# Performance work log

Measured on AMD Instinct MI355X. Metric: run time of the kernel, lower is better.

## Reference

```python
import jax, jax.numpy as jnp
import numpy as np

N_ATOMS = 4096
N_EDGES = 131072
NUM_BASIS = 8
CUTOFF = 6.0
EMBED = 64      # atom embedding dim
HID = 128       # hidden channel width
SH_DIM = 9      # l=0,1,2 spherical harmonics
TP_IN = HID * SH_DIM  # 1152
N_HEADS = 4
HEAD_DIM = HID // N_HEADS


def _spherical_harmonics(vec):
    # vec: [E,3] -> [E,9] matching the torch SphericalHarmonics (l=0,1,2)
    r = jnp.linalg.norm(vec, axis=-1, keepdims=True) + 1e-8
    u = vec / r
    x, y, z = u[:, 0], u[:, 1], u[:, 2]
    l0 = jnp.ones_like(x)[:, None]
    l1 = jnp.stack([y, z, x], axis=-1)
    l2 = jnp.stack([3.0 * z * z - 1.0, x * z, y * z, x * y, x * x - y * y], axis=-1)
    return jnp.concatenate([l0, l1, l2], axis=-1)


def _rbf(d):
    # bessel RBF with cosine cutoff, d: [E] -> [E, NUM_BASIS]
    freqs = jnp.arange(1, NUM_BASIS + 1, dtype=d.dtype) * (np.pi / CUTOFF)
    cut = 0.5 * (jnp.cos(d * (np.pi / CUTOFF)) + 1.0) * (d < CUTOFF).astype(d.dtype)
    rbf = jnp.sin(d[:, None] * freqs) / d[:, None]
    return rbf * cut[:, None]


def _mace_block(atomic_numbers, edge_index, edge_vectors, edge_lengths,
                atom_embed, rad_w1, rad_b1, rad_w2, rad_b2, tp_w, tp_b,
                msg_w1, msg_b1, msg_w2, msg_b2,
                attn_w_in, attn_b_in, attn_w_out, attn_b_out,
                gate_w, gate_b, out_w, out_b):
    n_atoms = atom_embed.shape[0] if False else atomic_numbers.shape[0]
    node = atom_embed[atomic_numbers]                      # [N,64] gather
    sh = _spherical_harmonics(edge_vectors)                # [E,9]
    rbf = _rbf(edge_lengths)                               # [E,8]
    rad = jax.nn.silu(rbf @ rad_w1 + rad_b1)
    rad = jax.nn.silu(rad @ rad_w2 + rad_b2)               # [E,128]
    # per-l outer products radial x sh_l, flattened channel-major, concatenated
    slices = [(0, 1), (1, 4), (4, 9)]
    msgs = jnp.concatenate(
        [(rad[:, :, None] * sh[:, None, s:e]).reshape(rad.shape[0], -1) for s, e in slices],
        axis=-1)                                           # [E,1152]
    edge_msg = msgs @ tp_w + tp_b                          # [E,128]
    dst = edge_index[1]
    agg = jax.ops.segment_sum(edge_msg, dst, num_segments=n_atoms)  # [N,128] scatter-add
    combined = jnp.concatenate([node, agg], axis=-1)       # [N,192]
    upd = jax.nn.silu(combined @ msg_w1 + msg_b1) @ msg_w2 + msg_b2  # [N,128]
    # multi-head self-attention over all atoms (batch of 1)
    qkv = upd @ attn_w_in.T + attn_b_in                    # [N,384]
    q, k, v = jnp.split(qkv, 3, axis=-1)
    q = q.reshape(-1, N_HEADS, HEAD_DIM)
    k = k.reshape(-1, N_HEADS, HEAD_DIM)
    v = v.reshape(-1, N_HEADS, HEAD_DIM)
    scores = jnp.einsum('nhd,mhd->hnm', q, k) / np.sqrt(HEAD_DIM)
    attn = jax.nn.softmax(scores, axis=-1)
    att = jnp.einsum('hnm,mhd->nhd', attn, v).reshape(-1, HID)
    att = att @ attn_w_out.T + attn_b_out                  # [N,128]
    gate = jax.nn.sigmoid(upd @ gate_w + gate_b)
    out = gate * att + (1.0 - gate) * upd
    return out @ out_w + out_b                             # [N,128]


def setup_inputs() -> dict:
    key = jax.random.key(0)
    ks = jax.random.split(key, 20)
    def w(k, shape, s=0.05):
        return jax.random.normal(k, shape, dtype=jnp.float32) * s
    return {
        'atomic_numbers': jax.random.randint(ks[0], (N_ATOMS,), 0, 100),
        'positions': jax.random.normal(ks[1], (N_ATOMS, 3), dtype=jnp.float32),
        'edge_index': jax.random.randint(ks[2], (2, N_EDGES), 0, N_ATOMS),
        'edge_vectors': jax.random.normal(ks[3], (N_EDGES, 3), dtype=jnp.float32),
        'edge_lengths': jax.random.uniform(ks[4], (N_EDGES,), dtype=jnp.float32, minval=0.5, maxval=5.9),
        'atom_embed': w(ks[5], (100, EMBED), 1.0),
        'rad_w1': w(ks[6], (NUM_BASIS, 64)), 'rad_b1': jnp.zeros((64,), jnp.float32),
        'rad_w2': w(ks[7], (64, HID)), 'rad_b2': jnp.zeros((HID,), jnp.float32),
        'tp_w': w(ks[8], (TP_IN, HID)), 'tp_b': jnp.zeros((HID,), jnp.float32),
        'msg_w1': w(ks[9], (EMBED + HID, HID)), 'msg_b1': jnp.zeros((HID,), jnp.float32),
        'msg_w2': w(ks[10], (HID, HID)), 'msg_b2': jnp.zeros((HID,), jnp.float32),
        'attn_w_in': w(ks[11], (3 * HID, HID)), 'attn_b_in': jnp.zeros((3 * HID,), jnp.float32),
        'attn_w_out': w(ks[12], (HID, HID)), 'attn_b_out': jnp.zeros((HID,), jnp.float32),
        'gate_w': w(ks[13], (HID, HID)), 'gate_b': jnp.zeros((HID,), jnp.float32),
        'out_w': w(ks[14], (HID, HID)), 'out_b': jnp.zeros((HID,), jnp.float32),
    }


def reference(atomic_numbers, positions, edge_index, edge_vectors, edge_lengths,
              atom_embed, rad_w1, rad_b1, rad_w2, rad_b2, tp_w, tp_b,
              msg_w1, msg_b1, msg_w2, msg_b2,
              attn_w_in, attn_b_in, attn_w_out, attn_b_out,
              gate_w, gate_b, out_w, out_b):
    # positions is accepted (as in the torch signature) but unused by the block math
    del positions
    return _mace_block(atomic_numbers, edge_index, edge_vectors, edge_lengths,
                       atom_embed, rad_w1, rad_b1, rad_w2, rad_b2, tp_w, tp_b,
                       msg_w1, msg_b1, msg_w2, msg_b2,
                       attn_w_in, attn_b_in, attn_w_out, attn_b_out,
                       gate_w, gate_b, out_w, out_b)
```

## Files before the change

### kernel.cpp

```cpp
#include <hip/hip_runtime.h>
#include <math.h>

#define N_ATOMS 4096
#define N_EDGES 131072
#define PI6 0.52359877559829887f
#define CAP 128

typedef __attribute__((ext_vector_type(8))) short bf16x8;
typedef __attribute__((ext_vector_type(4))) float f32x4;

#define MFMA(A,B,C) __builtin_amdgcn_mfma_f32_16x16x32_bf16((A),(B),(C),0,0,0)

__device__ __forceinline__ float silu_f(float x){ return x / (1.f + __expf(-x)); }
__device__ __forceinline__ float sigmoid_f(float x){ return 1.f / (1.f + __expf(-x)); }
__device__ __forceinline__ unsigned int f2bf(float f){
  unsigned int u = __float_as_uint(f);
  return (u + 0x7FFFu + ((u>>16)&1u)) >> 16;
}
__device__ __forceinline__ float bf2f(unsigned short h){
  return __uint_as_float(((unsigned int)h)<<16);
}
__device__ __forceinline__ bf16x8 ld8(const unsigned short* p){
  union { unsigned int u[4]; bf16x8 v; } r;
  const unsigned int* q = (const unsigned int*)p;
  r.u[0]=q[0]; r.u[1]=q[1]; r.u[2]=q[2]; r.u[3]=q[3];
  return r.v;
}
__device__ __forceinline__ void split_store(float v, unsigned short* ph, unsigned short* pl){
  unsigned int hb = f2bf(v);
  *ph = (unsigned short)hb;
  *pl = (unsigned short)f2bf(v - __uint_as_float(hb<<16));
}

__global__ __launch_bounds__(256) void prep_kernel(
  const float* __restrict__ attn_w_out, const float* __restrict__ rad_w2,
  const float* __restrict__ tp_w, const float* __restrict__ msg_w1,
  const float* __restrict__ msg_w2, const float* __restrict__ attn_w_in,
  const float* __restrict__ gate_w, const float* __restrict__ out_w,
  int* __restrict__ cursor,
  unsigned short* __restrict__ w2t_h, unsigned short* __restrict__ w2t_l,
  unsigned short* __restrict__ tpwT_h, unsigned short* __restrict__ tpwT_l,
  unsigned short* __restrict__ w1T_h, unsigned short* __restrict__ w1T_l,
  unsigned short* __restrict__ w2T_h, unsigned short* __restrict__ w2T_l,
  unsigned short* __restrict__ awin_h, unsigned short* __restrict__ awin_l,
  unsigned short* __restrict__ gwT_h, unsigned short* __restrict__ gwT_l,
  unsigned short* __restrict__ awo_h, unsigned short* __restrict__ awo_l,
  unsigned short* __restrict__ owT_h, unsigned short* __restrict__ owT_l)
{
  int idx = blockIdx.x*256 + threadIdx.x;
  if (idx < 4096) cursor[idx] = 0;
  if (idx < 8192){
    int j = idx; int k = j>>7, c = j&127;
    split_store(rad_w2[k*128+c], &w2t_h[c*64+k], &w2t_l[c*64+k]);
  } else if (idx < 155648){
    int j = idx - 8192; int col = j&127, kk = j>>7;
    int jj = kk>>7, c = kk&127;
    int r = (jj==0)? c : (jj<4 ? 128 + c*3 + (jj-1) : 512 + c*5 + (jj-4));
    split_store(tp_w[r*128+col], &tpwT_h[col*1152+kk], &tpwT_l[col*1152+kk]);
  } else if (idx < 180224){
    int j = idx - 155648; int col = j&127, k = j>>7;
    split_store(msg_w1[k*128+col], &w1T_h[col*192+k], &w1T_l[col*192+k]);
  } else if (idx < 196608){
    int j = idx - 180224; int col = j&127, k = j>>7;
    split_store(msg_w2[k*128+col], &w2T_h[col*128+k], &w2T_l[col*128+k]);
  } else if (idx < 245760){
    int j = idx - 196608;
    split_store(attn_w_in[j], &awin_h[j], &awin_l[j]);
  } else if (idx < 262144){
    int j = idx - 245760; int col = j&127, k = j>>7;
    split_store(gate_w[k*128+col], &gwT_h[col*128+k], &gwT_l[col*128+k]);
  } else if (idx < 278528){
    int j = idx - 262144;
    split_store(attn_w_out[j], &awo_h[j], &awo_l[j]);
  } else if (idx < 294912){
    int j = idx - 278528; int col = j&127, k = j>>7;
    split_store(out_w[k*128+col], &owT_h[col*128+k], &owT_l[col*128+k]);
  }
}

__global__ __launch_bounds__(256) void bucket_kernel(
  const int* __restrict__ edge_index, int* __restrict__ cursor, int* __restrict__ edge_slot)
{
  int e = blockIdx.x*256 + threadIdx.x;
  if (e < N_EDGES){
    int d = edge_index[N_EDGES + e];
    int pos = atomicAdd(&cursor[d], 1);
    if (pos < CAP) edge_slot[d*CAP + pos] = e;
  }
}

__global__ __launch_bounds__(512) void edge_F_kernel(
  const float* __restrict__ edge_vectors, const float* __restrict__ edge_lengths,
  const float* __restrict__ rad_w1, const float* __restrict__ rad_b1,
  const unsigned short* __restrict__ w2t_h, const unsigned short* __restrict__ w2t_l,
  const float* __restrict__ rad_b2,
  const int* __restrict__ cursor, const int* __restrict__ edge_slot,
  unsigned short* __restrict__ Fh, unsigned short* __restrict__ Fl)
{
  const int tid = threadIdx.x;
  const int w = tid >> 6, lane = tid & 63;
  const int l15 = lane & 15, lg = lane >> 4;
  const int wm = w >> 2, wn2 = w & 3;

  __shared__ unsigned short W1h[64][36],  W1l[64][36];
  __shared__ unsigned short RBh[32][36],  RBl[32][36];
  __shared__ unsigned short SHh[16][36],  SHl[16][36];
  __shared__ unsigned short R1h[32][72],  R1l[32][72];
  __shared__ unsigned short R2wh[8][16][34], R2wl[8][16][34];

  bf16x8 WAh[2], WAl[2];
  {
    int c = w*16 + l15;
    WAh[0] = ld8(&w2t_h[c*64 + lg*8]);
    WAh[1] = ld8(&w2t_h[c*64 + 32 + lg*8]);
    WAl[0] = ld8(&w2t_l[c*64 + lg*8]);
    WAl[1] = ld8(&w2t_l[c*64 + 32 + lg*8]);
  }

  for (int i = tid; i < 2048; i += 512){
    int c = i >> 5, k = i & 31;
    float v = (k < 8) ? rad_w1[k*64 + c] : 0.f;
    split_store(v, &W1h[c][k], &W1l[c][k]);
  }
  for (int i = tid; i < 32*36; i += 512){ RBh[i/36][i%36]=0; RBl[i/36][i%36]=0; }
  for (int i = tid; i < 16*36; i += 512){ SHh[i/36][i%36]=0; SHl[i/36][i%36]=0; }

  const float b1v = rad_b1[wn2*16 + l15];
  float b2r[4];
  #pragma unroll
  for (int r=0;r<4;r++) b2r[r] = rad_b2[w*16 + lg*4 + r];

  __syncthreads();

  for (int aa = 0; aa < 2; ++aa){
    const int a = blockIdx.x*2 + aa;
    const int deg = min(cursor[a], CAP);
    const int base = a*CAP;
    f32x4 facc = {0.f,0.f,0.f,0.f};

    for (int t0 = 0; t0 < deg; t0 += 32){
      if (tid < 256){
        int e8 = tid >> 3, k = tid & 7;
        int idx = t0 + e8;
        int eid = edge_slot[base + (idx < deg ? idx : 0)];
        float d = edge_lengths[eid];
        float cut = 0.5f*(__cosf(d*PI6)+1.f)*(d<6.f?1.f:0.f);
        float rb = __sinf(d*((float)(k+1)*PI6))/d*cut;
        if (idx >= deg) rb = 0.f;
        split_store(rb, &RBh[e8][k], &RBl[e8][k]);
      } else {
        int e8 = (tid-256) >> 3, u = tid & 7;
        int idx = t0 + e8;
        bool val = idx < deg;
        int eid = edge_slot[base + (val ? idx : 0)];
        float vx = edge_vectors[eid*3], vy = edge_vectors[eid*3+1], vz = edge_vectors[eid*3+2];
        float rn = sqrtf(vx*vx+vy*vy+vz*vz) + 1e-8f;
        float x = vx/rn, y = vy/rn, z = vz/rn;
        float sv;
        switch(u){
          case 0: sv = 1.f; break;
          case 1: sv = y; break;
          case 2: sv = z; break;
          case 3: sv = x; break;
          case 4: sv = 3.f*z*z-1.f; break;
          case 5: sv = x*z; break;
          case 6: sv = y*z; break;
          default: sv = x*y; break;
        }
        if (!val) sv = 0.f;
        split_store(sv, &SHh[u][e8], &SHl[u][e8]);
        if (u == 0){
          float s8 = val ? (x*x - y*y) : 0.f;
          split_store(s8, &SHh[8][e8], &SHl[8][e8]);
        }
      }
      __syncthreads();

      {
        bf16x8 Ah = ld8(&RBh[wm*16 + l15][lg*8]);
        bf16x8 Al = ld8(&RBl[wm*16 + l15][lg*8]);
        bf16x8 Bh = ld8(&W1h[wn2*16 + l15][lg*8]);
        bf16x8 Bl = ld8(&W1l[wn2*16 + l15][lg*8]);
        f32x4 z = {0.f,0.f,0.f,0.f};
        z = MFMA(Ah,Bl,z); z = MFMA(Al,Bh,z); z = MFMA(Ah,Bh,z);
        #pragma unroll
        for (int r=0;r<4;r++){
          int e8 = wm*16 + lg*4 + r;
          int c  = wn2*16 + l15;
          float v = silu_f(z[r] + b1v);
          split_store(v, &R1h[e8][c], &R1l[e8][c]);
        }
      }
      __syncthreads();

      #pragma unroll
      for (int et=0; et<2; et++){
        bf16x8 Bh0 = ld8(&R1h[et*16+l15][lg*8]);
        bf16x8 Bh1 = ld8(&R1h[et*16+l15][32+lg*8]);
        bf16x8 Bl0 = ld8(&R1l[et*16+l15][lg*8]);
        bf16x8 Bl1 = ld8(&R1l[et*16+l15][32+lg*8]);
        f32x4 z = {0.f,0.f,0.f,0.f};
        z = MFMA(WAl[0],Bh0,z); z = MFMA(WAl[1],Bh1,z);
        z = MFMA(WAh[0],Bl0,z); z = MFMA(WAh[1],Bl1,z);
        z = MFMA(WAh[0],Bh0,z); z = MFMA(WAh[1],Bh1,z);
        #pragma unroll
        for (int r=0;r<4;r++){
          float v = silu_f(z[r] + b2r[r]);
          split_store(v, &R2wh[w][lg*4+r][et*16+l15], &R2wl[w][lg*4+r][et*16+l15]);
        }
      }
      __asm__ volatile("s_waitcnt lgkmcnt(0)" ::: "memory");
      __builtin_amdgcn_sched_barrier(0);
      {
        bf16x8 Ah = ld8(&R2wh[w][l15][lg*8]);
        bf16x8 Al = ld8(&R2wl[w][l15][lg*8]);
        bf16x8 Bh = ld8(&SHh[l15][lg*8]);
        bf16x8 Bl = ld8(&SHl[l15][lg*8]);
        facc = MFMA(Ah,Bl,facc);
        facc = MFMA(Al,Bh,facc);
        facc = MFMA(Ah,Bh,facc);
      }
      __syncthreads();
    }

    if (l15 < 9){
      #pragma unroll
      for (int r=0;r<4;r++){
        int c = w*16 + lg*4 + r;
        size_t o = (size_t)l15*(N_ATOMS*128) + (size_t)a*128 + c;
        split_store(facc[r], &Fh[o], &Fl[o]);
      }
    }
  }
}

__global__ __launch_bounds__(512) void node_kernel(
  const int* __restrict__ atomic_numbers, const float* __restrict__ atom_embed,
  const unsigned short* __restrict__ Fh, const unsigned short* __restrict__ Fl,
  const unsigned short* __restrict__ tpwT_h, const unsigned short* __restrict__ tpwT_l,
  const float* __restrict__ tp_b, const int* __restrict__ cursor,
  const unsigned short* __restrict__ w1T_h, const unsigned short* __restrict__ w1T_l,
  const float* __restrict__ msg_b1,
  const unsigned short* __restrict__ w2T_h, const unsigned short* __restrict__ w2T_l,
  const float* __restrict__ msg_b2,
  const unsigned short* __restrict__ awin_h, const unsigned short* __restrict__ awin_l,
  const float* __restrict__ attn_b_in,
  unsigned short* __restrict__ updh, unsigned short* __restrict__ updl,
  unsigned short* __restrict__ Qbf, unsigned short* __restrict__ Kbf,
  unsigned short* __restrict__ Vtb)
{
  const int a0 = blockIdx.x*16, tid = threadIdx.x;
  const int w = tid>>6, lane = tid&63, l15 = lane&15, lg = lane>>4;

  __shared__ unsigned short Ch[16][200], Cl[16][200];
  __shared__ unsigned short Hh[16][136], Hl[16][136];
  __shared__ unsigned short Uh[16][136], Ul[16][136];

  for (int i=tid; i<1024; i+=512){
    int a16=i>>6, k=i&63;
    float v = atom_embed[atomic_numbers[a0+a16]*64+k];
    split_store(v, &Ch[a16][k], &Cl[a16][k]);
  }

  {
    f32x4 z = {0.f,0.f,0.f,0.f};
    for (int ch=0; ch<36; ch++){
      int k0=ch*32, j=k0>>7, c0=k0&127;
      size_t aoff = (size_t)j*(N_ATOMS*128) + (size_t)(a0+l15)*128 + c0 + lg*8;
      bf16x8 Ah=ld8(Fh+aoff), Al=ld8(Fl+aoff);
      size_t boff = (size_t)(w*16+l15)*1152 + k0 + lg*8;
      bf16x8 Bh=ld8(tpwT_h+boff), Bl=ld8(tpwT_l+boff);
      z = MFMA(Ah,Bl,z); z = MFMA(Al,Bh,z); z = MFMA(Ah,Bh,z);
    }
    int col = w*16+l15;
    float tb = tp_b[col];
    #pragma unroll
    for (int r=0;r<4;r++){
      int row = lg*4+r, arow = a0+row;
      float deg = (float)cursor[arow];
      float v = z[r] + tb*deg;
      split_store(v, &Ch[row][64+col], &Cl[row][64+col]);
    }
  }
  __syncthreads();

  {
    f32x4 z = {0.f,0.f,0.f,0.f};
    #pragma unroll
    for (int ch=0; ch<6; ch++){
      int k0=ch*32;
      bf16x8 Ah=ld8(&Ch[l15][k0+lg*8]), Al=ld8(&Cl[l15][k0+lg*8]);
      size_t boff=(size_t)(w*16+l15)*192 + k0 + lg*8;
      bf16x8 Bh=ld8(w1T_h+boff), Bl=ld8(w1T_l+boff);
      z = MFMA(Ah,Bl,z); z = MFMA(Al,Bh,z); z = MFMA(Ah,Bh,z);
    }
    int col = w*16+l15;
    float mb = msg_b1[col];
    #pragma unroll
    for (int r=0;r<4;r++){
      int row = lg*4+r;
      float v = silu_f(z[r]+mb);
      split_store(v, &Hh[row][col], &Hl[row][col]);
    }
  }
  __syncthreads();

  {
    f32x4 z = {0.f,0.f,0.f,0.f};
    #pragma unroll
    for (int ch=0; ch<4; ch++){
      int k0=ch*32;
      bf16x8 Ah=ld8(&Hh[l15][k0+lg*8]), Al=ld8(&Hl[l15][k0+lg*8]);
      size_t boff=(size_t)(w*16+l15)*128 + k0 + lg*8;
      bf16x8 Bh=ld8(w2T_h+boff), Bl=ld8(w2T_l+boff);
      z = MFMA(Ah,Bl,z); z = MFMA(Al,Bh,z); z = MFMA(Ah,Bh,z);
    }
    int col = w*16+l15;
    float mb = msg_b2[col];
    #pragma unroll
    for (int r=0;r<4;r++){
      int row = lg*4+r;
      float v = z[r]+mb;
      size_t o = (size_t)(a0+row)*128 + col;
      unsigned int hb = f2bf(v);
      updh[o] = (unsigned short)hb;
      float lo = v - __uint_as_float(hb<<16);
      updl[o] = (unsigned short)f2bf(lo);
      Uh[row][col] = (unsigned short)hb;
      Ul[row][col] = (unsigned short)f2bf(lo);
    }
  }
  __syncthreads();

  #pragma unroll
  for (int t3=0; t3<3; t3++){
    f32x4 z = {0.f,0.f,0.f,0.f};
    int col = (w*3+t3)*16 + l15;
    #pragma unroll
    for (int ch=0; ch<4; ch++){
      int k0=ch*32;
      bf16x8 Ah=ld8(&Uh[l15][k0+lg*8]), Al=ld8(&Ul[l15][k0+lg*8]);
      size_t boff=(size_t)col*128 + k0 + lg*8;
      bf16x8 Bh=ld8(awin_h+boff), Bl=ld8(awin_l+boff);
      z = MFMA(Ah,Bl,z); z = MFMA(Al,Bh,z); z = MFMA(Ah,Bh,z);
    }
    float ab = attn_b_in[col];
    int p = col>>7, hh = (col>>5)&3, dd = col&31;
    #pragma unroll
    for (int r=0;r<4;r++){
      int row = a0 + lg*4 + r;
      float v = z[r]+ab;
      if (p==0)      Qbf[(size_t)hh*131072 + (size_t)row*32 + dd] =
                       (unsigned short)f2bf(v*0.17677669529663687f);
      else if (p==1) Kbf[(size_t)hh*131072 + (size_t)row*32 + dd] = (unsigned short)f2bf(v);
      else           Vtb[(size_t)hh*131072 + (size_t)dd*4096 + row] = (unsigned short)f2bf(v);
    }
  }
}

__global__ __launch_bounds__(512) void attn_kernel(
  const unsigned short* __restrict__ Qbf, const unsigned short* __restrict__ Kbf,
  const unsigned short* __restrict__ Vtb,
  unsigned short* __restrict__ atth, unsigned short* __restrict__ attl)
{
  const int tid = threadIdx.x;
  const int w = tid>>6, lane = tid&63, l15 = lane&15, lg = lane>>4;
  const int qjl = w>>2, ks = w&3;
  const int qj = blockIdx.x*2 + qjl;
  const int h = qj >> 8, qt = qj & 255;

  __shared__ unsigned short Ps[8][16][72];
  __shared__ float MBo[2][4][16][32];
  __shared__ float MBm[2][4][16];
  __shared__ float MBs[2][4][16];

  const unsigned short* Kb = Kbf + (size_t)h*131072;
  const unsigned short* Vb = Vtb + (size_t)h*131072;

  bf16x8 bQ = ld8(&Qbf[(size_t)h*131072 + (size_t)(qt*16+l15)*32 + lg*8]);

  float m = -3e38f, su = 0.f;
  f32x4 oacc[2] = {{0.f,0.f,0.f,0.f},{0.f,0.f,0.f,0.f}};

  for (int kt = ks*16; kt < ks*16 + 16; ++kt){
    const int k0 = kt*64;
    f32x4 s[4];
    #pragma unroll
    for (int n=0;n<4;n++){
      bf16x8 aK = ld8(&Kb[(size_t)(k0+n*16+l15)*32 + lg*8]);
      f32x4 z = {0.f,0.f,0.f,0.f};
      s[n] = MFMA(aK, bQ, z);
    }
    float tmax = s[0][0];
    #pragma unroll
    for (int n=0;n<4;n++)
      #pragma unroll
      for (int r=0;r<4;r++) tmax = fmaxf(tmax, s[n][r]);
    tmax = fmaxf(tmax, __shfl_xor(tmax,16,64));
    tmax = fmaxf(tmax, __shfl_xor(tmax,32,64));
    float mn = fmaxf(m, tmax);
    float csc = __expf(m - mn);
    m = mn;
    float psum = 0.f;
    unsigned int* prow = (unsigned int*)&Ps[w][l15][0];
    #pragma unroll
    for (int n=0;n<4;n++){
      float p0=__expf(s[n][0]-mn), p1=__expf(s[n][1]-mn);
      float p2=__expf(s[n][2]-mn), p3=__expf(s[n][3]-mn);
      psum += (p0+p1)+(p2+p3);
      prow[n*8+lg*2]   = f2bf(p0) | (f2bf(p1)<<16);
      prow[n*8+lg*2+1] = f2bf(p2) | (f2bf(p3)<<16);
    }
    psum += __shfl_xor(psum,16,64);
    psum += __shfl_xor(psum,32,64);
    su = su*csc + psum;
    float cr[4];
    #pragma unroll
    for (int r=0;r<4;r++) cr[r] = __shfl(csc, lg*4+r, 64);
    #pragma unroll
    for (int nd=0;nd<2;nd++)
      #pragma unroll
      for (int r=0;r<4;r++) oacc[nd][r] *= cr[r];
    __asm__ volatile("s_waitcnt lgkmcnt(0)" ::: "memory");
    #pragma unroll
    for (int kc=0;kc<2;kc++){
      bf16x8 aP = ld8(&Ps[w][l15][kc*32 + lg*8]);
      #pragma unroll
      for (int nd=0;nd<2;nd++){
        bf16x8 bV = ld8(&Vb[(size_t)(nd*16+l15)*4096 + k0 + kc*32 + lg*8]);
        oacc[nd] = MFMA(aP, bV, oacc[nd]);
      }
    }
  }

  if (lg==0){ MBm[qjl][ks][l15]=m; MBs[qjl][ks][l15]=su; }
  #pragma unroll
  for (int nd=0;nd<2;nd++)
    #pragma unroll
    for (int r=0;r<4;r++) MBo[qjl][ks][lg*4+r][nd*16+l15] = oacc[nd][r];
  __syncthreads();

  for (int idx = tid; idx < 1024; idx += 512){
    int qq = idx>>9, q = (idx>>5)&15, d = idx&31;
    float m0=MBm[qq][0][q], m1=MBm[qq][1][q], m2=MBm[qq][2][q], m3=MBm[qq][3][q];
    float mf = fmaxf(fmaxf(m0,m1), fmaxf(m2,m3));
    float c0=__expf(m0-mf), c1=__expf(m1-mf), c2=__expf(m2-mf), c3=__expf(m3-mf);
    float st = MBs[qq][0][q]*c0 + MBs[qq][1][q]*c1 + MBs[qq][2][q]*c2 + MBs[qq][3][q]*c3;
    float o  = MBo[qq][0][q][d]*c0 + MBo[qq][1][q][d]*c1 + MBo[qq][2][q][d]*c2 + MBo[qq][3][q][d]*c3;
    int qj2 = blockIdx.x*2 + qq;
    int hh = qj2>>8, qrow = (qj2&255)*16 + q;
    size_t off = (size_t)qrow*128 + hh*32 + d;
    split_store(o/st, &atth[off], &attl[off]);
  }
}

__global__ __launch_bounds__(512) void final_kernel(
  const unsigned short* __restrict__ atth, const unsigned short* __restrict__ attl,
  const unsigned short* __restrict__ updh, const unsigned short* __restrict__ updl,
  const unsigned short* __restrict__ awo_h, const unsigned short* __restrict__ awo_l,
  const float* __restrict__ attn_b_out,
  const unsigned short* __restrict__ gwT_h, const unsigned short* __restrict__ gwT_l,
  const float* __restrict__ gate_b,
  const unsigned short* __restrict__ owT_h, const unsigned short* __restrict__ owT_l,
  const float* __restrict__ out_b,
  float* __restrict__ out)
{
  const int a0 = blockIdx.x*16, tid = threadIdx.x;
  const int w = tid>>6, lane = tid&63, l15 = lane&15, lg = lane>>4;

  __shared__ unsigned short Th[16][136], Tl[16][136];

  const int col = w*16 + l15;

  f32x4 za = {0.f,0.f,0.f,0.f};
  f32x4 zg = {0.f,0.f,0.f,0.f};
  #pragma unroll
  for (int ch=0; ch<4; ch++){
    int k0=ch*32;
    size_t aoff = (size_t)(a0+l15)*128 + k0 + lg*8;
    bf16x8 Aah=ld8(atth+aoff), Aal=ld8(attl+aoff);
    bf16x8 Auh=ld8(updh+aoff), Aul=ld8(updl+aoff);
    size_t boff=(size_t)col*128 + k0 + lg*8;
    bf16x8 Bah=ld8(awo_h+boff), Bal=ld8(awo_l+boff);
    bf16x8 Bgh=ld8(gwT_h+boff), Bgl=ld8(gwT_l+boff);
    za = MFMA(Aah,Bal,za); za = MFMA(Aal,Bah,za); za = MFMA(Aah,Bah,za);
    zg = MFMA(Auh,Bgl,zg); zg = MFMA(Aul,Bgh,zg); zg = MFMA(Auh,Bgh,zg);
  }
  {
    float ab = attn_b_out[col], gb = gate_b[col];
    #pragma unroll
    for (int r=0;r<4;r++){
      int row = lg*4+r;
      size_t uo = (size_t)(a0+row)*128 + col;
      float uv = bf2f(updh[uo]) + bf2f(updl[uo]);
      float g = sigmoid_f(zg[r]+gb);
      float t = g*(za[r]+ab) + (1.f-g)*uv;
      split_store(t, &Th[row][col], &Tl[row][col]);
    }
  }
  __syncthreads();

  f32x4 zo = {0.f,0.f,0.f,0.f};
  #pragma unroll
  for (int ch=0; ch<4; ch++){
    int k0=ch*32;
    bf16x8 Ah=ld8(&Th[l15][k0+lg*8]), Al=ld8(&Tl[l15][k0+lg*8]);
    size_t boff=(size_t)col*128 + k0 + lg*8;
    bf16x8 Bh=ld8(owT_h+boff), Bl=ld8(owT_l+boff);
    zo = MFMA(Ah,Bl,zo); zo = MFMA(Al,Bh,zo); zo = MFMA(Ah,Bh,zo);
  }
  {
    float ob = out_b[col];
    #pragma unroll
    for (int r=0;r<4;r++){
      int row = lg*4+r;
      out[(size_t)(a0+row)*128 + col] = zo[r] + ob;
    }
  }
}

extern "C" void kernel_launch(void* const* d_in, const int* in_sizes, int n_in,
                              void* d_out, int out_size, void* d_ws, size_t ws_size,
                              hipStream_t stream){
  const int*   atomic_numbers = (const int*)  d_in[0];
  const int*   edge_index     = (const int*)  d_in[2];
  const float* edge_vectors   = (const float*)d_in[3];
  const float* edge_lengths   = (const float*)d_in[4];
  const float* atom_embed     = (const float*)d_in[5];
  const float* rad_w1 = (const float*)d_in[6];
  const float* rad_b1 = (const float*)d_in[7];
  const float* rad_w2 = (const float*)d_in[8];
  const float* rad_b2 = (const float*)d_in[9];
  const float* tp_w   = (const float*)d_in[10];
  const float* tp_b   = (const float*)d_in[11];
  const float* msg_w1 = (const float*)d_in[12];
  const float* msg_b1 = (const float*)d_in[13];
  const float* msg_w2 = (const float*)d_in[14];
  const float* msg_b2 = (const float*)d_in[15];
  const float* attn_w_in  = (const float*)d_in[16];
  const float* attn_b_in  = (const float*)d_in[17];
  const float* attn_w_out = (const float*)d_in[18];
  const float* attn_b_out = (const float*)d_in[19];
  const float* gate_w = (const float*)d_in[20];
  const float* gate_b = (const float*)d_in[21];
  const float* out_w  = (const float*)d_in[22];
  const float* out_b  = (const float*)d_in[23];

  char* ws = (char*)d_ws;
  int* cursor    = (int*)(ws);
  int* edge_slot = (int*)(ws + 16384);
  unsigned short* w2t_h  = (unsigned short*)(ws + 2113536);
  unsigned short* w2t_l  = (unsigned short*)(ws + 2129920);
  unsigned short* tpwT_h = (unsigned short*)(ws + 2146304);
  unsigned short* tpwT_l = (unsigned short*)(ws + 2441216);
  unsigned short* w1T_h  = (unsigned short*)(ws + 2736128);
  unsigned short* w1T_l  = (unsigned short*)(ws + 2785280);
  unsigned short* w2T_h  = (unsigned short*)(ws + 2834432);
  unsigned short* w2T_l  = (unsigned short*)(ws + 2867200);
  unsigned short* awin_h = (unsigned short*)(ws + 2899968);
  unsigned short* awin_l = (unsigned short*)(ws + 2998272);
  unsigned short* gwT_h  = (unsigned short*)(ws + 3096576);
  unsigned short* gwT_l  = (unsigned short*)(ws + 3129344);
  unsigned short* awo_h  = (unsigned short*)(ws + 3162112);
  unsigned short* awo_l  = (unsigned short*)(ws + 3194880);
  unsigned short* owT_h  = (unsigned short*)(ws + 3227648);
  unsigned short* owT_l  = (unsigned short*)(ws + 3260416);
  unsigned short* Fbf_h  = (unsigned short*)(ws + 3293184);
  unsigned short* Fbf_l  = (unsigned short*)(ws + 12730368);
  unsigned short* atth   = (unsigned short*)(ws + 3293184);
  unsigned short* attl   = (unsigned short*)(ws + 4341760);
  unsigned short* updh   = (unsigned short*)(ws + 22167552);
  unsigned short* updl   = (unsigned short*)(ws + 23216128);
  unsigned short* Qbf    = (unsigned short*)(ws + 24264704);
  unsigned short* Kbf    = (unsigned short*)(ws + 25313280);
  unsigned short* Vtb    = (unsigned short*)(ws + 26361856);

  prep_kernel<<<1152, 256, 0, stream>>>(attn_w_out, rad_w2, tp_w, msg_w1, msg_w2,
      attn_w_in, gate_w, out_w, cursor,
      w2t_h, w2t_l, tpwT_h, tpwT_l, w1T_h, w1T_l, w2T_h, w2T_l, awin_h, awin_l,
      gwT_h, gwT_l, awo_h, awo_l, owT_h, owT_l);
  bucket_kernel<<<(N_EDGES+255)/256, 256, 0, stream>>>(edge_index, cursor, edge_slot);
  edge_F_kernel<<<N_ATOMS/2, 512, 0, stream>>>(edge_vectors, edge_lengths,
      rad_w1, rad_b1, w2t_h, w2t_l, rad_b2, cursor, edge_slot, Fbf_h, Fbf_l);
  node_kernel<<<N_ATOMS/16, 512, 0, stream>>>(atomic_numbers, atom_embed,
      Fbf_h, Fbf_l, tpwT_h, tpwT_l, tp_b, cursor,
      w1T_h, w1T_l, msg_b1, w2T_h, w2T_l, msg_b2, awin_h, awin_l, attn_b_in,
      updh, updl, Qbf, Kbf, Vtb);
  attn_kernel<<<512, 512, 0, stream>>>(Qbf, Kbf, Vtb, atth, attl);
  final_kernel<<<N_ATOMS/16, 512, 0, stream>>>(atth, attl, updh, updl,
      awo_h, awo_l, attn_b_out, gwT_h, gwT_l, gate_b, owT_h, owT_l, out_b,
      (float*)d_out);
}
```

Measured before the change: 176.5 us.

## Software-pipeline edge data loads across flattened two-atom chunk loop

Flattens the per-block two-atom loop into a single loop over 32-edge chunks and prefetches the next chunk's edge slot, length and vector loads while the current chunk's RBF/SH and MFMA work proceeds. The global gather latency that previously sat on the critical path before each barrier is meant to be hidden. In exchange it keeps extra registers live for the prefetched values and adds more complex per-chunk indexing and output-write logic.

```diff
diff --git a/kernel.cpp b/kernel.cpp
--- a/kernel.cpp
+++ b/kernel.cpp
@@ -130,108 +130,150 @@
   #pragma unroll
   for (int r=0;r<4;r++) b2r[r] = rad_b2[w*16 + lg*4 + r];
 
+  const int a0 = blockIdx.x*2;
+  const int deg0 = min(cursor[a0], CAP), deg1 = min(cursor[a0+1], CAP);
+  const int c0 = (deg0+31)>>5, c1 = (deg1+31)>>5;
+  const int nc = c0 + c1;
+
+  const bool isRB = (tid < 256);
+  const int ht = isRB ? tid : tid-256;
+  const int e8 = ht >> 3, u = ht & 7;
+
+  #define CHUNK_PARAMS(i, t0v, degv, basev) { \
+    int ia_ = ((i) < c0) ? 0 : 1; \
+    t0v = (((i) < c0) ? (i) : ((i)-c0)) << 5; \
+    degv = ia_ ? deg1 : deg0; \
+    basev = (a0 + ia_)*CAP; }
+
+  #define WRITE_F(atomid) \
+    if (l15 < 9){ \
+      _Pragma("unroll") \
+      for (int r_=0;r_<4;r_++){ \
+        int c_ = w*16 + lg*4 + r_; \
+        size_t o_ = (size_t)l15*(N_ATOMS*128) + (size_t)(atomid)*128 + c_; \
+        split_store(facc[r_], &Fh[o_], &Fl[o_]); \
+      } }
+
+  f32x4 facc = {0.f,0.f,0.f,0.f};
+
+  if (c0 == 0){ WRITE_F(a0) }
+  if (c1 == 0){ WRITE_F(a0+1) }
+
+  int eid_c = 0; float d_c = 1.f, vx_c = 0.f, vy_c = 0.f, vz_c = 1.f;
+  if (nc > 0){
+    int t0v, degv, basev; CHUNK_PARAMS(0, t0v, degv, basev);
+    int idx = t0v + e8;
+    eid_c = edge_slot[basev + (idx < degv ? idx : 0)];
+    if (isRB) d_c = edge_lengths[eid_c];
+    else { vx_c = edge_vectors[eid_c*3]; vy_c = edge_vectors[eid_c*3+1]; vz_c = edge_vectors[eid_c*3+2]; }
+  }
+
   __syncthreads();
 
-  for (int aa = 0; aa < 2; ++aa){
-    const int a = blockIdx.x*2 + aa;
-    const int deg = min(cursor[a], CAP);
-    const int base = a*CAP;
-    f32x4 facc = {0.f,0.f,0.f,0.f};
-
-    for (int t0 = 0; t0 < deg; t0 += 32){
-      if (tid < 256){
-        int e8 = tid >> 3, k = tid & 7;
-        int idx = t0 + e8;
-        int eid = edge_slot[base + (idx < deg ? idx : 0)];
-        float d = edge_lengths[eid];
-        float cut = 0.5f*(__cosf(d*PI6)+1.f)*(d<6.f?1.f:0.f);
-        float rb = __sinf(d*((float)(k+1)*PI6))/d*cut;
-        if (idx >= deg) rb = 0.f;
-        split_store(rb, &RBh[e8][k], &RBl[e8][k]);
-      } else {
-        int e8 = (tid-256) >> 3, u = tid & 7;
-        int idx = t0 + e8;
-        bool val = idx < deg;
-        int eid = edge_slot[base + (val ? idx : 0)];
-        float vx = edge_vectors[eid*3], vy = edge_vectors[eid*3+1], vz = edge_vectors[eid*3+2];
-        float rn = sqrtf(vx*vx+vy*vy+vz*vz) + 1e-8f;
-        float x = vx/rn, y = vy/rn, z = vz/rn;
-        float sv;
-        switch(u){
-          case 0: sv = 1.f; break;
-          case 1: sv = y; break;
-          case 2: sv = z; break;
-          case 3: sv = x; break;
-          case 4: sv = 3.f*z*z-1.f; break;
-          case 5: sv = x*z; break;
-          case 6: sv = y*z; break;
-          default: sv = x*y; break;
-        }
-        if (!val) sv = 0.f;
-        split_store(sv, &SHh[u][e8], &SHl[u][e8]);
-        if (u == 0){
-          float s8 = val ? (x*x - y*y) : 0.f;
-          split_store(s8, &SHh[8][e8], &SHl[8][e8]);
-        }
+  for (int i = 0; i < nc; ++i){
+    int t0v, degv, basev; CHUNK_PARAMS(i, t0v, degv, basev);
+    const bool val = (t0v + e8) < degv;
+
+    const bool hn = (i+1) < nc;
+    int eid_n = 0;
+    if (hn){
+      int t0n, degn, basen; CHUNK_PARAMS(i+1, t0n, degn, basen);
+      int idxn = t0n + e8;
+      eid_n = edge_slot[basen + (idxn < degn ? idxn : 0)];
+    }
+
+    if (isRB){
+      float cut = 0.5f*(__cosf(d_c*PI6)+1.f)*(d_c<6.f?1.f:0.f);
+      float rb = __sinf(d_c*((float)(u+1)*PI6))/d_c*cut;
+      if (!val) rb = 0.f;
+      split_store(rb, &RBh[e8][u], &RBl[e8][u]);
+    } else {
+      float rn = sqrtf(vx_c*vx_c+vy_c*vy_c+vz_c*vz_c) + 1e-8f;
+      float x = vx_c/rn, y = vy_c/rn, z = vz_c/rn;
+      float sv;
+      switch(u){
+        case 0: sv = 1.f; break;
+        case 1: sv = y; break;
+        case 2: sv = z; break;
+        case 3: sv = x; break;
+        case 4: sv = 3.f*z*z-1.f; break;
+        case 5: sv = x*z; break;
+        case 6: sv = y*z; break;
+        default: sv = x*y; break;
       }
-      __syncthreads();
-
-      {
-        bf16x8 Ah = ld8(&RBh[wm*16 + l15][lg*8]);
-        bf16x8 Al = ld8(&RBl[wm*16 + l15][lg*8]);
-        bf16x8 Bh = ld8(&W1h[wn2*16 + l15][lg*8]);
-        bf16x8 Bl = ld8(&W1l[wn2*16 + l15][lg*8]);
-        f32x4 z = {0.f,0.f,0.f,0.f};
-        z = MFMA(Ah,Bl,z); z = MFMA(Al,Bh,z); z = MFMA(Ah,Bh,z);
-        #pragma unroll
-        for (int r=0;r<4;r++){
-          int e8 = wm*16 + lg*4 + r;
-          int c  = wn2*16 + l15;
-          float v = silu_f(z[r] + b1v);
-          split_store(v, &R1h[e8][c], &R1l[e8][c]);
-        }
+      if (!val) sv = 0.f;
+      split_store(sv, &SHh[u][e8], &SHl[u][e8]);
+      if (u == 0){
+        float s8 = val ? (x*x - y*y) : 0.f;
+        split_store(s8, &SHh[8][e8], &SHl[8][e8]);
       }
-      __syncthreads();
-
-      #pragma unroll
-      for (int et=0; et<2; et++){
-        bf16x8 Bh0 = ld8(&R1h[et*16+l15][lg*8]);
-        bf16x8 Bh1 = ld8(&R1h[et*16+l15][32+lg*8]);
-        bf16x8 Bl0 = ld8(&R1l[et*16+l15][lg*8]);
-        bf16x8 Bl1 = ld8(&R1l[et*16+l15][32+lg*8]);
-        f32x4 z = {0.f,0.f,0.f,0.f};
-        z = MFMA(WAl[0],Bh0,z); z = MFMA(WAl[1],Bh1,z);
-        z = MFMA(WAh[0],Bl0,z); z = MFMA(WAh[1],Bl1,z);
-        z = MFMA(WAh[0],Bh0,z); z = MFMA(WAh[1],Bh1,z);
-        #pragma unroll
-        for (int r=0;r<4;r++){
-          float v = silu_f(z[r] + b2r[r]);
-          split_store(v, &R2wh[w][lg*4+r][et*16+l15], &R2wl[w][lg*4+r][et*16+l15]);
-        }
-      }
-      __asm__ volatile("s_waitcnt lgkmcnt(0)" ::: "memory");
-      __builtin_amdgcn_sched_barrier(0);
-      {
-        bf16x8 Ah = ld8(&R2wh[w][l15][lg*8]);
-        bf16x8 Al = ld8(&R2wl[w][l15][lg*8]);
-        bf16x8 Bh = ld8(&SHh[l15][lg*8]);
-        bf16x8 Bl = ld8(&SHl[l15][lg*8]);
-        facc = MFMA(Ah,Bl,facc);
-        facc = MFMA(Al,Bh,facc);
-        facc = MFMA(Ah,Bh,facc);
-      }
-      __syncthreads();
-    }
-
-    if (l15 < 9){
+    }
+
+    float d_n = 1.f, vx_n = 0.f, vy_n = 0.f, vz_n = 1.f;
+    if (hn){
+      if (isRB) d_n = edge_lengths[eid_n];
+      else { vx_n = edge_vectors[eid_n*3]; vy_n = edge_vectors[eid_n*3+1]; vz_n = edge_vectors[eid_n*3+2]; }
+    }
+    __syncthreads();
+
+    {
+      bf16x8 Ah = ld8(&RBh[wm*16 + l15][lg*8]);
+      bf16x8 Al = ld8(&RBl[wm*16 + l15][lg*8]);
+      bf16x8 Bh = ld8(&W1h[wn2*16 + l15][lg*8]);
+      bf16x8 Bl = ld8(&W1l[wn2*16 + l15][lg*8]);
+      f32x4 z = {0.f,0.f,0.f,0.f};
+      z = MFMA(Ah,Bl,z); z = MFMA(Al,Bh,z); z = MFMA(Ah,Bh,z);
       #pragma unroll
       for (int r=0;r<4;r++){
-        int c = w*16 + lg*4 + r;
-        size_t o = (size_t)l15*(N_ATOMS*128) + (size_t)a*128 + c;
-        split_store(facc[r], &Fh[o], &Fl[o]);
+        int ee = wm*16 + lg*4 + r;
+        int c  = wn2*16 + l15;
+        float v = silu_f(z[r] + b1v);
+        split_store(v, &R1h[ee][c], &R1l[ee][c]);
       }
     }
-  }
+    __syncthreads();
+
+    #pragma unroll
+    for (int et=0; et<2; et++){
+      bf16x8 Bh0 = ld8(&R1h[et*16+l15][lg*8]);
+      bf16x8 Bh1 = ld8(&R1h[et*16+l15][32+lg*8]);
+      bf16x8 Bl0 = ld8(&R1l[et*16+l15][lg*8]);
+      bf16x8 Bl1 = ld8(&R1l[et*16+l15][32+lg*8]);
+      f32x4 z = {0.f,0.f,0.f,0.f};
+      z = MFMA(WAl[0],Bh0,z); z = MFMA(WAl[1],Bh1,z);
+      z = MFMA(WAh[0],Bl0,z); z = MFMA(WAh[1],Bl1,z);
+      z = MFMA(WAh[0],Bh0,z); z = MFMA(WAh[1],Bh1,z);
+      #pragma unroll
+      for (int r=0;r<4;r++){
+        float v = silu_f(z[r] + b2r[r]);
+        split_store(v, &R2wh[w][lg*4+r][et*16+l15], &R2wl[w][lg*4+r][et*16+l15]);
+      }
+    }
+    __asm__ volatile("s_waitcnt lgkmcnt(0)" ::: "memory");
+    __builtin_amdgcn_sched_barrier(0);
+    {
+      bf16x8 Ah = ld8(&R2wh[w][l15][lg*8]);
+      bf16x8 Al = ld8(&R2wl[w][l15][lg*8]);
+      bf16x8 Bh = ld8(&SHh[l15][lg*8]);
+      bf16x8 Bl = ld8(&SHl[l15][lg*8]);
+      facc = MFMA(Ah,Bl,facc);
+      facc = MFMA(Al,Bh,facc);
+      facc = MFMA(Ah,Bh,facc);
+    }
+    __syncthreads();
+
+    if (i == c0-1){
+      WRITE_F(a0)
+      facc = (f32x4){0.f,0.f,0.f,0.f};
+    }
+    if (i == nc-1 && c1 > 0){
+      WRITE_F(a0+1)
+    }
+
+    eid_c = eid_n; d_c = d_n; vx_c = vx_n; vy_c = vy_n; vz_c = vz_n;
+  }
+  #undef CHUNK_PARAMS
+  #undef WRITE_F
 }
 
 __global__ __launch_bounds__(512) void node_kernel(
```

After: 184.5 us. 1.05x slower.
